# Performance work log

Hardware: AMD Instinct MI355X
Metric: run time of the kernel (lower is better)

## Reference

```python
import jax, jax.numpy as jnp
import numpy as np

N_NODES = 50000; N_INTRA = 800000; N_INTER = 400000; N_IEDGE = 600000
N_GRAPHS = 128; F_IN = 54; DIM = 128; N_GNN = 3; DIM_MLP = 128
DEV_VDW_COEFF = 0.2; EPS_LO = 0.0178; EPS_HI = 0.2
VDW_N_SHORT = 10.0; VDW_N_LONG = 6.0
RANGE_LO = 0.5; RANGE_HI = 5.0
HBOND_CUT = (-0.7, 0.0); METAL_CUT = (-0.7, 0.0); HYDRO_CUT = (0.5, 1.5)


def _lin(key, fi, fo):
    return jax.random.normal(key, (fi, fo), jnp.float32) / np.float32(np.sqrt(fi))


def setup_inputs():
    key = jax.random.key(0)
    ks = iter(jax.random.split(key, 48))
    nk = lambda: next(ks)
    inp = {}
    inp['x'] = jax.random.normal(nk(), (N_NODES, F_IN), jnp.float32)
    inp['pos'] = jax.random.uniform(nk(), (N_NODES, 3), jnp.float32, 0.0, 20.0)
    inp['vdw_radii'] = jax.random.uniform(nk(), (N_NODES,), jnp.float32, 1.0, 2.0)
    inp['rotor'] = jax.random.randint(nk(), (N_GRAPHS, 1), 0, 20).astype(jnp.float32)
    inp['edge_index'] = jax.random.randint(nk(), (2, N_INTRA), 0, N_NODES)
    inp['edge_index_c'] = jax.random.randint(nk(), (2, N_INTER), 0, N_NODES)
    inp['edge_index_i'] = jax.random.randint(nk(), (2, N_IEDGE), 0, N_NODES)
    inp['batch'] = jnp.sort(jax.random.randint(nk(), (N_NODES,), 0, N_GRAPHS))
    for name, p in (('is_metal', 0.02), ('is_h_donor', 0.15), ('is_h_acceptor', 0.2), ('is_hydrophobic', 0.4)):
        inp[name] = jax.random.bernoulli(nk(), p, (N_NODES,))
    inp['embed_W'] = _lin(nk(), F_IN, DIM)
    inp['gat_W'] = jax.random.normal(nk(), (N_GNN, DIM, DIM), jnp.float32) / np.float32(np.sqrt(DIM))
    inp['gat_Wb'] = jnp.zeros((N_GNN, DIM), jnp.float32)
    inp['gat_A'] = 0.1 * jax.random.normal(nk(), (N_GNN, DIM, DIM), jnp.float32) / np.float32(np.sqrt(DIM))
    inp['gat_gate_w'] = jax.random.normal(nk(), (N_GNN, 2 * DIM, 1), jnp.float32) / np.float32(np.sqrt(2 * DIM))
    inp['gat_gate_b'] = jnp.zeros((N_GNN, 1), jnp.float32)
    inp['inter_W'] = jax.random.normal(nk(), (N_GNN, DIM, DIM), jnp.float32) / np.float32(np.sqrt(DIM))
    inp['inter_Wb'] = jnp.zeros((N_GNN, DIM), jnp.float32)
    inp['inter_gate_w'] = jax.random.normal(nk(), (N_GNN, 2 * DIM, 1), jnp.float32) / np.float32(np.sqrt(2 * DIM))
    inp['inter_gate_b'] = jnp.zeros((N_GNN, 1), jnp.float32)
    inp['eps_w1'] = _lin(nk(), 2 * DIM, DIM_MLP); inp['eps_b1'] = jnp.zeros((DIM_MLP,), jnp.float32)
    inp['eps_w2'] = _lin(nk(), DIM_MLP, 1); inp['eps_b2'] = jnp.zeros((1,), jnp.float32)
    inp['dvdw_w1'] = _lin(nk(), 2 * DIM, DIM_MLP); inp['dvdw_b1'] = jnp.zeros((DIM_MLP,), jnp.float32)
    inp['dvdw_w2'] = _lin(nk(), DIM_MLP, 1); inp['dvdw_b2'] = jnp.zeros((1,), jnp.float32)
    inp['hbond_coeff'] = jnp.array([1.0], jnp.float32)
    inp['hydrophobic_coeff'] = jnp.array([0.5], jnp.float32)
    inp['rotor_coeff'] = jnp.array([0.5], jnp.float32)
    return inp


def _gated_gat(x, src, dst, W, Wb, A, gw, gb):
    n = x.shape[0]
    h = x @ W + Wb                                   # [N, D]
    logits = jnp.sum((h @ A)[dst] * h[src], axis=-1)  # per-edge attention logit
    mx = jax.ops.segment_max(logits, dst, num_segments=n)
    mx = jnp.where(jnp.isfinite(mx), mx, 0.0)
    ex = jnp.exp(logits - mx[dst])
    den = jax.ops.segment_sum(ex, dst, num_segments=n)
    alpha = ex / (den[dst] + 1e-16)                  # segment softmax over incoming edges
    h_prime = jax.nn.relu(jax.ops.segment_sum(alpha[:, None] * h[src], dst, num_segments=n))
    z = jax.nn.sigmoid(jnp.concatenate([x, h_prime], -1) @ gw + gb)
    return z * x + (1.0 - z) * h_prime


def _interaction(x, src, dst, W, Wb, gw, gb):
    n = x.shape[0]
    m = jax.ops.segment_sum(jax.nn.relu(x[src] @ W + Wb), dst, num_segments=n)
    z = jax.nn.sigmoid(jnp.concatenate([x, m], -1) @ gw + gb)
    return z * x + (1.0 - z) * m


def _lj(D, R, eps, n_short, n_long):
    dr = jnp.maximum(D / R, 0.5)  # numerical clamp mirroring PIGNet's distance clamp
    n = jnp.where(dr < 1.0, n_short, n_long)
    return eps * (dr ** (-2.0 * n) - 2.0 * dr ** (-n))


def _linear_potential(D, R, minima, c_short, c_long):
    frac = jnp.clip(((D - R) - c_long) / (c_short - c_long), 0.0, 1.0)
    return minima * frac


def _forward(x, pos, vdw_radii, rotor, embed_W, gat_W, gat_Wb, gat_A, gat_gate_w, gat_gate_b,
             inter_W, inter_Wb, inter_gate_w, inter_gate_b,
             eps_w1, eps_b1, eps_w2, eps_b2, dvdw_w1, dvdw_b1, dvdw_w2, dvdw_b2,
             hbond_coeff, hydrophobic_coeff, rotor_coeff,
             edge_index, edge_index_c, edge_index_i, batch,
             is_metal, is_h_donor, is_h_acceptor, is_hydrophobic):
    h = x @ embed_W
    for l in range(N_GNN):
        h = _gated_gat(h, edge_index[0], edge_index[1], gat_W[l], gat_Wb[l], gat_A[l], gat_gate_w[l], gat_gate_b[l])
    for l in range(N_GNN):
        h = _interaction(h, edge_index_c[0], edge_index_c[1], inter_W[l], inter_Wb[l], inter_gate_w[l], inter_gate_b[l])
    i, j = edge_index_i[0], edge_index_i[1]
    diff = pos[i] - pos[j]
    D = jnp.sqrt(jnp.sum(diff * diff, axis=-1) + 1e-10)           # [E]
    rmask = ((D >= RANGE_LO) & (D <= RANGE_HI)).astype(h.dtype)
    x_cat = jnp.concatenate([h[i], h[j]], axis=-1)                # [E, 2*DIM]
    dvdw = jnp.tanh(jax.nn.relu(x_cat @ dvdw_w1 + dvdw_b1) @ dvdw_w2 + dvdw_b2)[:, 0]
    dvdw = dvdw * DEV_VDW_COEFF * rmask
    R = vdw_radii[i] + vdw_radii[j] + dvdw
    eps = jax.nn.sigmoid(jax.nn.relu(x_cat @ eps_w1 + eps_b1) @ eps_w2 + eps_b2)[:, 0]
    eps = eps * (EPS_HI - EPS_LO) + EPS_LO
    min_hb = -hbond_coeff ** 2
    min_hp = -hydrophobic_coeff ** 2
    e = jnp.stack([
        _lj(D, R, eps, VDW_N_SHORT, VDW_N_LONG),
        _linear_potential(D, R, min_hb, *HBOND_CUT),
        _linear_potential(D, R, min_hb, *METAL_CUT),
        _linear_potential(D, R, min_hp, *HYDRO_CUT),
    ])                                                            # [4, E]
    no_metal = ~(is_metal[i] | is_metal[j])
    masks = jnp.stack([
        no_metal,
        ((is_h_donor[i] & is_h_acceptor[j]) | (is_h_acceptor[i] & is_h_donor[j])) & no_metal,
        (is_metal[i] & is_h_acceptor[j]) | (is_h_acceptor[i] & is_metal[j]),
        is_hydrophobic[i] & is_hydrophobic[j] & no_metal,
    ]).astype(e.dtype)
    e = e * masks * rmask
    energies = jax.ops.segment_sum(e.T, batch[i], num_segments=N_GRAPHS)  # [G, 4]
    penalty = 1.0 + rotor_coeff ** 2 * rotor                               # [G, 1]
    return energies / penalty, dvdw


def reference(x, pos, vdw_radii, rotor, edge_index, edge_index_c, edge_index_i, batch,
              is_metal, is_h_donor, is_h_acceptor, is_hydrophobic,
              embed_W, gat_W, gat_Wb, gat_A, gat_gate_w, gat_gate_b,
              inter_W, inter_Wb, inter_gate_w, inter_gate_b,
              eps_w1, eps_b1, eps_w2, eps_b2, dvdw_w1, dvdw_b1, dvdw_w2, dvdw_b2,
              hbond_coeff, hydrophobic_coeff, rotor_coeff):
    return _forward(x, pos, vdw_radii, rotor, embed_W, gat_W, gat_Wb, gat_A, gat_gate_w, gat_gate_b,
                    inter_W, inter_Wb, inter_gate_w, inter_gate_b,
                    eps_w1, eps_b1, eps_w2, eps_b2, dvdw_w1, dvdw_b1, dvdw_w2, dvdw_b2,
                    hbond_coeff, hydrophobic_coeff, rotor_coeff,
                    edge_index, edge_index_c, edge_index_i, batch,
                    is_metal, is_h_donor, is_h_acceptor, is_hydrophobic)
```

## Files before the change

### kernel.cpp

```cpp
#include <hip/hip_runtime.h>
#include <math.h>

#define NN 50000
#define EA 800000
#define EC 400000
#define EIN 600000
#define NG 128
#define FIN 54

#define DEV_VDW 0.2f
#define EPS_LO_ 0.0178f
#define EPS_HI_ 0.2f

typedef unsigned int uint;
typedef unsigned short ushort;
typedef __attribute__((ext_vector_type(8))) short bf16x8;
typedef __attribute__((ext_vector_type(4))) float f32x4;

__device__ __forceinline__ ushort f2bf(float f){
  uint x = __float_as_uint(f);
  uint r = x + 0x7fffu + ((x >> 16) & 1u);
  return (ushort)(r >> 16);
}
__device__ __forceinline__ uint f2bf2(float a, float b){
  return (uint)f2bf(a) | ((uint)f2bf(b) << 16);
}
__device__ __forceinline__ void decode8(uint4 u, float* f){
  f[0] = __uint_as_float(u.x << 16); f[1] = __uint_as_float(u.x & 0xffff0000u);
  f[2] = __uint_as_float(u.y << 16); f[3] = __uint_as_float(u.y & 0xffff0000u);
  f[4] = __uint_as_float(u.z << 16); f[5] = __uint_as_float(u.z & 0xffff0000u);
  f[6] = __uint_as_float(u.w << 16); f[7] = __uint_as_float(u.w & 0xffff0000u);
}

__global__ void k_count2(const int* __restrict__ dstA, const int* __restrict__ dstC,
                         int* __restrict__ cntA, int* __restrict__ cntC){
  int half = blockIdx.x >= 1024;
  const int* dst = half ? dstC : dstA;
  int* cnt = half ? cntC : cntA;
  int E = half ? EC : EA;
  int bid = blockIdx.x - (half ? 1024 : 0);
  int i = bid * 256 + threadIdx.x;
  for (; i < E; i += 1024 * 256) atomicAdd(&cnt[dst[i]], 1);
}

__global__ void k_scan2(const int* __restrict__ cntA, int* __restrict__ offA, int* __restrict__ curA,
                        const int* __restrict__ cntC, int* __restrict__ offC, int* __restrict__ curC){
  const int* cnt = blockIdx.x ? cntC : cntA;
  int* off = blockIdx.x ? offC : offA;
  int* cur = blockIdx.x ? curC : curA;
  int n = NN;
  __shared__ int wsums[16];
  __shared__ int run_s;
  int tid = threadIdx.x;
  int lane = tid & 63, w = tid >> 6;
  if (tid == 0) run_s = 0;
  __syncthreads();
  for (int base = 0; base < n; base += 1024){
    int run = run_s;
    int i = base + tid;
    int v = (i < n) ? cnt[i] : 0;
    int s = v;
    #pragma unroll
    for (int o = 1; o < 64; o <<= 1){ int t = __shfl_up(s, o, 64); if (lane >= o) s += t; }
    if (lane == 63) wsums[w] = s;
    __syncthreads();
    if (w == 0 && lane < 16){
      int t = wsums[lane];
      #pragma unroll
      for (int o = 1; o < 16; o <<= 1){ int u = __shfl_up(t, o, 64); if (lane >= o) t += u; }
      wsums[lane] = t;
    }
    __syncthreads();
    int woff = (w == 0) ? 0 : wsums[w - 1];
    int excl = run + woff + (s - v);
    if (i < n){ off[i] = excl; cur[i] = excl; }
    int tot = wsums[15];
    __syncthreads();
    if (tid == 0) run_s = run + tot;
    __syncthreads();
  }
  if (threadIdx.x == 0) off[n] = run_s;
}

__global__ void k_place2(const int* __restrict__ eiA, const int* __restrict__ eiC,
                         int* __restrict__ curA, int* __restrict__ srcA,
                         int* __restrict__ curC, int* __restrict__ srcC){
  int half = blockIdx.x >= 1024;
  const int* src = half ? eiC : eiA;
  const int* dst = half ? eiC + EC : eiA + EA;
  int* cur = half ? curC : curA;
  int* outp = half ? srcC : srcA;
  int E = half ? EC : EA;
  int bid = blockIdx.x - (half ? 1024 : 0);
  int i = bid * 256 + threadIdx.x;
  for (; i < E; i += 1024 * 256){
    int d = dst[i];
    int slot = atomicAdd(&cur[d], 1);
    outp[slot] = src[i];
  }
}

__global__ void k_nodeinfo(const float* __restrict__ POS, const float* __restrict__ RAD,
                           const int* __restrict__ Mmet, const int* __restrict__ Mdon,
                           const int* __restrict__ Macc, const int* __restrict__ Mhyd,
                           const int* __restrict__ BATCH,
                           float4* __restrict__ PRAD, uint* __restrict__ MB){
  int n = blockIdx.x * 256 + threadIdx.x;
  if (n < NN){
    PRAD[n] = make_float4(POS[3*n], POS[3*n+1], POS[3*n+2], RAD[n]);
    uint m = (Mmet[n] ? 1u : 0u) | (Mdon[n] ? 2u : 0u) | (Macc[n] ? 4u : 0u) |
             (Mhyd[n] ? 8u : 0u) | ((uint)BATCH[n] << 8);
    MB[n] = m;
  }
}

__global__ __launch_bounds__(256) void k_prepw(const float* __restrict__ gatW, const float* __restrict__ gatA,
                        const float* __restrict__ intW, const float* __restrict__ dw1,
                        const float* __restrict__ ew1,
                        const float* __restrict__ gatWb, const float* __restrict__ intWb,
                        const float* __restrict__ db1, const float* __restrict__ eb1,
                        uint* __restrict__ Wt, float* __restrict__ BIASALL){
  __shared__ ushort L[128 * 132];
  int m = blockIdx.x;
  int tid = threadIdx.x;
  if (m == 13){
    for (int idx = tid; idx < 13 * 128; idx += 256){
      int slot = idx >> 7, c = idx & 127;
      if (slot >= 3 && slot < 6) continue;
      float v = 0.f;
      if (slot < 3) v = gatWb[slot * 128 + c];
      else if (slot < 9) v = intWb[(slot - 6) * 128 + c];
      else if (slot == 9) v = db1[c];
      else if (slot == 11) v = eb1[c];
      BIASALL[idx] = v;
    }
    return;
  }
  if (m >= 3 && m < 6){
    int l = m - 3;
    const float* Wf  = gatW + l * 16384;
    const float* Af  = gatA + l * 16384;
    const float* Wbf = gatWb + l * 128;
    for (int idx = tid; idx < 16384; idx += 256){
      int k = idx >> 7, n = idx & 127;
      L[k * 132 + n] = f2bf(Af[idx]);
    }
    __syncthreads();
    int r = tid >> 1, ch = tid & 1;
    float accv[64];
    #pragma unroll
    for (int c = 0; c < 64; ++c) accv[c] = 0.f;
    float accb = 0.f;
    int bc = tid & 127;
    for (int mm = 0; mm < 128; ++mm){
      float wv = Wf[r * 128 + mm];
      const uint* Lr32 = (const uint*)&L[mm * 132 + ch * 64];
      #pragma unroll
      for (int c2 = 0; c2 < 32; ++c2){
        uint u = Lr32[c2];
        accv[2 * c2]     += wv * __uint_as_float(u << 16);
        accv[2 * c2 + 1] += wv * __uint_as_float(u & 0xffff0000u);
      }
      accb += Wbf[mm] * __uint_as_float((uint)L[mm * 132 + bc] << 16);
    }
    __syncthreads();
    #pragma unroll
    for (int c = 0; c < 64; ++c) L[r * 132 + ch * 64 + c] = f2bf(accv[c]);
    if (tid < 128) BIASALL[(3 + l) * 128 + tid] = accb;
    __syncthreads();
    int n = tid & 127, half = tid >> 7;
    uint* outp = Wt + (size_t)m * 8192 + n * 64 + half * 32;
    #pragma unroll
    for (int kk2 = 0; kk2 < 32; ++kk2){
      int k = half * 64 + 2 * kk2;
      uint u = (uint)L[k * 132 + n] | ((uint)L[(k + 1) * 132 + n] << 16);
      outp[kk2] = u;
    }
    return;
  }
  const float* src = (m < 3)  ? gatW + m * 16384 :
                     (m < 9)  ? intW + (m - 6) * 16384 :
                     (m < 11) ? dw1 + (m - 9) * 16384 :
                                ew1 + (m - 11) * 16384;
  for (int idx = tid; idx < 16384; idx += 256){
    int k = idx >> 7, n = idx & 127;
    L[k * 132 + n] = f2bf(src[idx]);
  }
  __syncthreads();
  int n = tid & 127, half = tid >> 7;
  uint* outp = Wt + (size_t)m * 8192 + n * 64 + half * 32;
  #pragma unroll
  for (int kk2 = 0; kk2 < 32; ++kk2){
    int k = half * 64 + 2 * kk2;
    uint u = (uint)L[k * 132 + n] | ((uint)L[(k + 1) * 132 + n] << 16);
    outp[kk2] = u;
  }
}

__global__ void k_embed(const float* __restrict__ X, const float* __restrict__ W,
                        float* __restrict__ H, uint* __restrict__ Hh){
  __shared__ float Wls[FIN * 128];
  int tid = threadIdx.x;
  for (int i = tid; i < FIN * 128; i += 128) Wls[i] = W[i];
  __syncthreads();
  for (int row = blockIdx.x; row < NN; row += gridDim.x){
    const float* xr = X + row * FIN;
    float acc = 0.f;
    #pragma unroll
    for (int k = 0; k < FIN; ++k) acc += xr[k] * Wls[k * 128 + tid];
    H[(size_t)row * 128 + tid] = acc;
    ((ushort*)Hh)[(size_t)row * 128 + tid] = f2bf(acc);
  }
}

template<bool RELU>
__global__ __launch_bounds__(256) void k_gemm_mfma(const uint* __restrict__ Ah,
        const uint* __restrict__ Bt0, size_t strideB,
        const float* __restrict__ bias0, size_t strideBias,
        uint* __restrict__ C0, size_t strideC, int N){
  const uint* Bt = Bt0 + (size_t)blockIdx.y * strideB;
  const float* bias = bias0 + (size_t)blockIdx.y * strideBias;
  uint* Cout = C0 + (size_t)blockIdx.y * strideC;
  int tid = threadIdx.x;
  int lane = tid & 63;
  int wv = tid >> 6;
  int row0 = blockIdx.x * 128 + wv * 32;
  int l15 = lane & 15, lg = lane >> 4;
  int ra0 = row0 + l15, ra1 = row0 + 16 + l15;
  const uint* pa0 = Ah + (size_t)(ra0 < N ? ra0 : 0) * 64 + lg * 4;
  const uint* pa1 = Ah + (size_t)(ra1 < N ? ra1 : 0) * 64 + lg * 4;
  const uint* pb  = Bt + (size_t)l15 * 64 + lg * 4;
  f32x4 acc[2][8] = {};
  #pragma unroll
  for (int c = 0; c < 4; ++c){
    bf16x8 a0 = *(const bf16x8*)(pa0 + c * 16);
    bf16x8 a1 = *(const bf16x8*)(pa1 + c * 16);
    #pragma unroll
    for (int ct = 0; ct < 8; ++ct){
      bf16x8 b = *(const bf16x8*)(pb + ct * 1024 + c * 16);
      acc[0][ct] = __builtin_amdgcn_mfma_f32_16x16x32_bf16(a0, b, acc[0][ct], 0, 0, 0);
      acc[1][ct] = __builtin_amdgcn_mfma_f32_16x16x32_bf16(a1, b, acc[1][ct], 0, 0, 0);
    }
  }
  #pragma unroll
  for (int ct = 0; ct < 8; ++ct){
    int col = ct * 16 + l15;
    float bv = bias[col];
    #pragma unroll
    for (int rt = 0; rt < 2; ++rt){
      int rbase = row0 + rt * 16 + lg * 4;
      f32x4 a4 = acc[rt][ct];
      #pragma unroll
      for (int r = 0; r < 4; ++r){
        int row = rbase + r;
        if (row < N){
          float t = a4[r] + bv;
          if (RELU) t = fmaxf(t, 0.f);
          ((ushort*)Cout)[(size_t)row * 128 + col] = f2bf(t);
        }
      }
    }
  }
}

__global__ __launch_bounds__(256) void k_gat(float* __restrict__ H, uint* __restrict__ Hh,
                      const uint* __restrict__ HWh, const uint* __restrict__ HAh,
                      const int* __restrict__ off, const int* __restrict__ srcs,
                      const float* __restrict__ GW, const float* __restrict__ GB){
  int tid = threadIdx.x;
  int n = blockIdx.x * 4 + (tid >> 6);
  if (n >= NN) return;
  int lane = tid & 63;
  int sub = lane & 15;
  int grp = lane >> 4;
  uint4 au = *(const uint4*)(HAh + (size_t)n * 64 + sub * 4);
  float a[8]; decode8(au, a);
  int e0 = off[n], deg = off[n + 1] - e0;
  float m = -1e30f, den = 0.f;
  float acc[8] = {};
  int slot = grp;
  bool act = slot < deg;
  int sv = (sub == 0 && act) ? srcs[e0 + slot] : 0;
  int s = __shfl(sv, lane & 48);
  uint4 wu = {};
  if (act) wu = *(const uint4*)(HWh + (size_t)s * 64 + sub * 4);
  int nit = (deg + 3) >> 2;
  for (int t = 0; t < nit; ++t){
    int slotn = slot + 4;
    bool actn = slotn < deg;
    int svn = (sub == 0 && actn) ? srcs[e0 + slotn] : 0;
    int sn = __shfl(svn, lane & 48);
    uint4 wun = {};
    if (actn) wun = *(const uint4*)(HWh + (size_t)sn * 64 + sub * 4);
    float w[8]; decode8(wu, w);
    float p = a[0]*w[0] + a[1]*w[1] + a[2]*w[2] + a[3]*w[3]
            + a[4]*w[4] + a[5]*w[5] + a[6]*w[6] + a[7]*w[7];
    #pragma unroll
    for (int o = 8; o; o >>= 1) p += __shfl_xor(p, o, 64);
    if (act){
      float mn = fmaxf(m, p);
      float cf = __expf(m - mn);
      float ex = __expf(p - mn);
      den = den * cf + ex;
      #pragma unroll
      for (int q = 0; q < 8; ++q) acc[q] = acc[q] * cf + ex * w[q];
      m = mn;
    }
    slot = slotn; act = actn; wu = wun;
  }
  #pragma unroll
  for (int o = 16; o <= 32; o <<= 1){
    float mo  = __shfl_xor(m, o, 64);
    float dno = __shfl_xor(den, o, 64);
    float ao[8];
    #pragma unroll
    for (int q = 0; q < 8; ++q) ao[q] = __shfl_xor(acc[q], o, 64);
    float mn = fmaxf(m, mo);
    float cf = __expf(m - mn), cfo = __expf(mo - mn);
    den = den * cf + dno * cfo;
    #pragma unroll
    for (int q = 0; q < 8; ++q) acc[q] = acc[q] * cf + ao[q] * cfo;
    m = mn;
  }
  float inv = 1.f / (den + 1e-16f);
  float hp[8];
  #pragma unroll
  for (int q = 0; q < 8; ++q) hp[q] = fmaxf(acc[q] * inv, 0.f);
  float x[8];
  *(float4*)&x[0] = *(const float4*)(H + (size_t)n * 128 + sub * 8);
  *(float4*)&x[4] = *(const float4*)(H + (size_t)n * 128 + sub * 8 + 4);
  float gx[8], gh[8];
  *(float4*)&gx[0] = *(const float4*)(GW + sub * 8);
  *(float4*)&gx[4] = *(const float4*)(GW + sub * 8 + 4);
  *(float4*)&gh[0] = *(const float4*)(GW + 128 + sub * 8);
  *(float4*)&gh[4] = *(const float4*)(GW + 128 + sub * 8 + 4);
  float g = 0.f;
  #pragma unroll
  for (int q = 0; q < 8; ++q) g += x[q] * gx[q] + hp[q] * gh[q];
  #pragma unroll
  for (int o = 8; o; o >>= 1) g += __shfl_xor(g, o, 64);
  g += GB[0];
  float z = 1.f / (1.f + __expf(-g));
  #pragma unroll
  for (int q = 0; q < 8; ++q) x[q] = z * x[q] + (1.f - z) * hp[q];
  if (grp == 0){
    *(float4*)(H + (size_t)n * 128 + sub * 8)     = *(float4*)&x[0];
    *(float4*)(H + (size_t)n * 128 + sub * 8 + 4) = *(float4*)&x[4];
    uint4 hw;
    hw.x = f2bf2(x[0], x[1]); hw.y = f2bf2(x[2], x[3]);
    hw.z = f2bf2(x[4], x[5]); hw.w = f2bf2(x[6], x[7]);
    *(uint4*)(Hh + (size_t)n * 64 + sub * 4) = hw;
  }
}

__global__ __launch_bounds__(256) void k_inter(float* __restrict__ H, uint* __restrict__ Hh,
                        const uint* __restrict__ Th,
                        const int* __restrict__ off, const int* __restrict__ srcs,
                        const float* __restrict__ GW, const float* __restrict__ GB){
  int tid = threadIdx.x;
  int n = blockIdx.x * 4 + (tid >> 6);
  if (n >= NN) return;
  int lane = tid & 63;
  int sub = lane & 15;
  int grp = lane >> 4;
  int e0 = off[n], deg = off[n + 1] - e0;
  float acc[8] = {};
  int slot = grp;
  bool act = slot < deg;
  int sv = (sub == 0 && act) ? srcs[e0 + slot] : 0;
  int s = __shfl(sv, lane & 48);
  uint4 wu = {};
  if (act) wu = *(const uint4*)(Th + (size_t)s * 64 + sub * 4);
  int nit = (deg + 3) >> 2;
  for (int t = 0; t < nit; ++t){
    int slotn = slot + 4;
    bool actn = slotn < deg;
    int svn = (sub == 0 && actn) ? srcs[e0 + slotn] : 0;
    int sn = __shfl(svn, lane & 48);
    uint4 wun = {};
    if (actn) wun = *(const uint4*)(Th + (size_t)sn * 64 + sub * 4);
    if (act){
      float w[8]; decode8(wu, w);
      #pragma unroll
      for (int q = 0; q < 8; ++q) acc[q] += w[q];
    }
    slot = slotn; act = actn; wu = wun;
  }
  #pragma unroll
  for (int q = 0; q < 8; ++q){
    acc[q] += __shfl_xor(acc[q], 16, 64);
    acc[q] += __shfl_xor(acc[q], 32, 64);
  }
  float x[8];
  *(float4*)&x[0] = *(const float4*)(H + (size_t)n * 128 + sub * 8);
  *(float4*)&x[4] = *(const float4*)(H + (size_t)n * 128 + sub * 8 + 4);
  float gx[8], gh[8];
  *(float4*)&gx[0] = *(const float4*)(GW + sub * 8);
  *(float4*)&gx[4] = *(const float4*)(GW + sub * 8 + 4);
  *(float4*)&gh[0] = *(const float4*)(GW + 128 + sub * 8);
  *(float4*)&gh[4] = *(const float4*)(GW + 128 + sub * 8 + 4);
  float g = 0.f;
  #pragma unroll
  for (int q = 0; q < 8; ++q) g += x[q] * gx[q] + acc[q] * gh[q];
  #pragma unroll
  for (int o = 8; o; o >>= 1) g += __shfl_xor(g, o, 64);
  g += GB[0];
  float z = 1.f / (1.f + __expf(-g));
  #pragma unroll
  for (int q = 0; q < 8; ++q) x[q] = z * x[q] + (1.f - z) * acc[q];
  if (grp == 0){
    *(float4*)(H + (size_t)n * 128 + sub * 8)     = *(float4*)&x[0];
    *(float4*)(H + (size_t)n * 128 + sub * 8 + 4) = *(float4*)&x[4];
    uint4 hw;
    hw.x = f2bf2(x[0], x[1]); hw.y = f2bf2(x[2], x[3]);
    hw.z = f2bf2(x[4], x[5]); hw.w = f2bf2(x[6], x[7]);
    *(uint4*)(Hh + (size_t)n * 64 + sub * 4) = hw;
  }
}

__global__ __launch_bounds__(256) void k_edges(
    const int* __restrict__ EI,
    const float4* __restrict__ PRAD, const uint* __restrict__ MB,
    const uint* __restrict__ Pd, const uint* __restrict__ Qd,
    const uint* __restrict__ Pe, const uint* __restrict__ Qe,
    const float* __restrict__ w2d, const float* __restrict__ b2d,
    const float* __restrict__ w2e, const float* __restrict__ b2e,
    const float* __restrict__ hbc, const float* __restrict__ hpc,
    float* __restrict__ geng, float* __restrict__ outdv){
  __shared__ float eg[NG * 4];
  int tid = threadIdx.x;
  for (int i = tid; i < NG * 4; i += 256) eg[i] = 0.f;
  __syncthreads();
  int sub = tid & 15;
  int gid = blockIdx.x * 16 + (tid >> 4);
  int ngrp = gridDim.x * 16;
  float wdv[8], wev[8];
  *(float4*)&wdv[0] = *(const float4*)(w2d + sub * 8);
  *(float4*)&wdv[4] = *(const float4*)(w2d + sub * 8 + 4);
  *(float4*)&wev[0] = *(const float4*)(w2e + sub * 8);
  *(float4*)&wev[4] = *(const float4*)(w2e + sub * 8 + 4);
  float bd = b2d[0], be = b2e[0];
  float minhb = -hbc[0] * hbc[0], minhp = -hpc[0] * hpc[0];

  int e = gid;
  uint4 pd0 = {}, qd0 = {}, pe0 = {}, qe0 = {};
  float4 pri0 = {}, prj0 = {};
  uint mbi0 = 0, mbj0 = 0;
  int i1 = 0, j1 = 0;
  if (e < EIN){
    int i0 = EI[e], j0 = EI[EIN + e];
    pd0 = *(const uint4*)(Pd + (size_t)i0 * 64 + sub * 4);
    qd0 = *(const uint4*)(Qd + (size_t)j0 * 64 + sub * 4);
    pe0 = *(const uint4*)(Pe + (size_t)i0 * 64 + sub * 4);
    qe0 = *(const uint4*)(Qe + (size_t)j0 * 64 + sub * 4);
    pri0 = PRAD[i0]; prj0 = PRAD[j0]; mbi0 = MB[i0]; mbj0 = MB[j0];
  }
  if (e + ngrp < EIN){ i1 = EI[e + ngrp]; j1 = EI[EIN + e + ngrp]; }

  for (; e < EIN; e += ngrp){
    uint4 pd1 = {}, qd1 = {}, pe1 = {}, qe1 = {};
    float4 pri1 = {}, prj1 = {};
    uint mbi1 = 0, mbj1 = 0;
    int i2 = 0, j2 = 0;
    if (e + ngrp < EIN){
      pd1 = *(const uint4*)(Pd + (size_t)i1 * 64 + sub * 4);
      qd1 = *(const uint4*)(Qd + (size_t)j1 * 64 + sub * 4);
      pe1 = *(const uint4*)(Pe + (size_t)i1 * 64 + sub * 4);
      qe1 = *(const uint4*)(Qe + (size_t)j1 * 64 + sub * 4);
      pri1 = PRAD[i1]; prj1 = PRAD[j1]; mbi1 = MB[i1]; mbj1 = MB[j1];
    }
    if (e + 2 * ngrp < EIN){ i2 = EI[e + 2 * ngrp]; j2 = EI[EIN + e + 2 * ngrp]; }

    float pdf[8], qdf[8], pef[8], qef[8];
    decode8(pd0, pdf); decode8(qd0, qdf); decode8(pe0, pef); decode8(qe0, qef);
    float sd = 0.f, se = 0.f;
    #pragma unroll
    for (int q = 0; q < 8; ++q){
      sd += fmaxf(pdf[q] + qdf[q], 0.f) * wdv[q];
      se += fmaxf(pef[q] + qef[q], 0.f) * wev[q];
    }
    #pragma unroll
    for (int o = 8; o; o >>= 1){
      sd += __shfl_xor(sd, o, 64);
      se += __shfl_xor(se, o, 64);
    }
    sd += bd; se += be;
    float dx = pri0.x - prj0.x, dy = pri0.y - prj0.y, dz = pri0.z - prj0.z;
    float D = sqrtf(dx * dx + dy * dy + dz * dz + 1e-10f);
    float rmask = (D >= 0.5f && D <= 5.0f) ? 1.f : 0.f;
    float ex2 = __expf(2.f * fminf(sd, 15.f));
    float th = __fdividef(ex2 - 1.f, ex2 + 1.f);
    float dvdw = th * DEV_VDW * rmask;
    float eps = __fdividef(1.f, 1.f + __expf(-se)) * (EPS_HI_ - EPS_LO_) + EPS_LO_;
    float R = pri0.w + prj0.w + dvdw;
    float dr = fmaxf(__fdividef(D, R), 0.5f);
    float nn2 = (dr < 1.f) ? 10.f : 6.f;
    float tp = __expf(-nn2 * __logf(dr));
    float ev = eps * (tp * tp - 2.f * tp);
    float dmr = D - R;
    float f1 = fminf(fmaxf(dmr * (-1.f / 0.7f), 0.f), 1.f);
    float f3 = fminf(fmaxf(1.5f - dmr, 0.f), 1.f);
    bool metI = mbi0 & 1, metJ = mbj0 & 1;
    bool donI = mbi0 & 2, donJ = mbj0 & 2;
    bool accI = mbi0 & 4, accJ = mbj0 & 4;
    bool hyI  = mbi0 & 8, hyJ  = mbj0 & 8;
    bool nm = !(metI || metJ);
    float E0 = nm ? ev * rmask : 0.f;
    float E1 = (((donI && accJ) || (accI && donJ)) && nm) ? minhb * f1 * rmask : 0.f;
    float E2 = ((metI && accJ) || (accI && metJ)) ? minhb * f1 * rmask : 0.f;
    float E3 = (hyI && hyJ && nm) ? minhp * f3 * rmask : 0.f;
    if (sub == 0){
      outdv[e] = dvdw;
      int g = (int)(mbi0 >> 8) * 4;
      atomicAdd(&eg[g + 0], E0);
      atomicAdd(&eg[g + 1], E1);
      atomicAdd(&eg[g + 2], E2);
      atomicAdd(&eg[g + 3], E3);
    }
    pd0 = pd1; qd0 = qd1; pe0 = pe1; qe0 = qe1;
    pri0 = pri1; prj0 = prj1; mbi0 = mbi1; mbj0 = mbj1;
    i1 = i2; j1 = j2;
  }
  __syncthreads();
  float* part = geng + (size_t)(blockIdx.x & 7) * (NG * 4);
  for (int i2 = tid; i2 < NG * 4; i2 += 256) atomicAdd(&part[i2], eg[i2]);
}

__global__ void k_final(const float* __restrict__ geng, const float* __restrict__ rotor,
                        const float* __restrict__ rc, float* __restrict__ out){
  int t = blockIdx.x * blockDim.x + threadIdx.x;
  if (t < NG * 4){
    int g = t >> 2;
    float s = 0.f;
    #pragma unroll
    for (int p = 0; p < 8; ++p) s += geng[p * NG * 4 + t];
    float pen = 1.f + rc[0] * rc[0] * rotor[g];
    out[t] = s / pen;
  }
}

extern "C" void kernel_launch(void* const* d_in, const int* in_sizes, int n_in,
                              void* d_out, int out_size, void* d_ws, size_t ws_size,
                              hipStream_t stream){
  (void)in_sizes; (void)n_in; (void)out_size; (void)ws_size;
  const float* X    = (const float*)d_in[0];
  const float* POS  = (const float*)d_in[1];
  const float* RAD  = (const float*)d_in[2];
  const float* ROT  = (const float*)d_in[3];
  const int* EIa    = (const int*)d_in[4];
  const int* EIc    = (const int*)d_in[5];
  const int* EIi    = (const int*)d_in[6];
  const int* BATCH  = (const int*)d_in[7];
  const int* Mmet = (const int*)d_in[8];
  const int* Mdon = (const int*)d_in[9];
  const int* Macc = (const int*)d_in[10];
  const int* Mhyd = (const int*)d_in[11];
  const float* embW  = (const float*)d_in[12];
  const float* gatW  = (const float*)d_in[13];
  const float* gatWb = (const float*)d_in[14];
  const float* gatA  = (const float*)d_in[15];
  const float* gatGw = (const float*)d_in[16];
  const float* gatGb = (const float*)d_in[17];
  const float* intW  = (const float*)d_in[18];
  const float* intWb = (const float*)d_in[19];
  const float* intGw = (const float*)d_in[20];
  const float* intGb = (const float*)d_in[21];
  const float* ew1 = (const float*)d_in[22];
  const float* eb1 = (const float*)d_in[23];
  const float* ew2 = (const float*)d_in[24];
  const float* eb2 = (const float*)d_in[25];
  const float* dw1 = (const float*)d_in[26];
  const float* db1 = (const float*)d_in[27];
  const float* dw2 = (const float*)d_in[28];
  const float* db2 = (const float*)d_in[29];
  const float* hbc = (const float*)d_in[30];
  const float* hpc = (const float*)d_in[31];
  const float* rcc = (const float*)d_in[32];
  float* out = (float*)d_out;

  char* w = (char*)d_ws;
  float* H   = (float*)w; w += (size_t)NN * 128 * 4;
  uint* Hh   = (uint*)w;  w += (size_t)NN * 64 * 4;
  uint* BAh  = (uint*)w;  w += (size_t)NN * 64 * 4;
  uint* BBh  = (uint*)w;  w += (size_t)NN * 64 * 4;
  uint* Peh  = (uint*)w;  w += (size_t)NN * 64 * 4;
  uint* Qeh  = (uint*)w;  w += (size_t)NN * 64 * 4;
  uint* WT   = (uint*)w;  w += (size_t)13 * 8192 * 4;
  float* BIASALL = (float*)w; w += (size_t)13 * 128 * 4;
  float4* PRAD = (float4*)w; w += (size_t)NN * 16;
  uint* MBb  = (uint*)w;  w += (size_t)NN * 4;
  float* GENG = (float*)w; w += (size_t)8 * 512 * 4;
  int* cntA = (int*)w; w += (size_t)NN * 4;
  int* offA = (int*)w; w += (size_t)(NN + 1) * 4;
  int* curA = (int*)w; w += (size_t)NN * 4;
  int* srcA = (int*)w; w += (size_t)EA * 4;
  int* cntC = (int*)w; w += (size_t)NN * 4;
  int* offC = (int*)w; w += (size_t)(NN + 1) * 4;
  int* curC = (int*)w; w += (size_t)NN * 4;
  int* srcC = (int*)w; w += (size_t)EC * 4;
  uint* Th  = BAh;
  uint* Pdh = BAh;
  uint* Qdh = BBh;

  hipMemsetAsync(cntA, 0, (size_t)NN * 4, stream);
  hipMemsetAsync(cntC, 0, (size_t)NN * 4, stream);
  hipMemsetAsync(GENG, 0, (size_t)8 * 512 * 4, stream);

  k_count2<<<2048, 256, 0, stream>>>(EIa + EA, EIc + EC, cntA, cntC);
  k_scan2<<<2, 1024, 0, stream>>>(cntA, offA, curA, cntC, offC, curC);
  k_place2<<<2048, 256, 0, stream>>>(EIa, EIc, curA, srcA, curC, srcC);

  k_prepw<<<14, 256, 0, stream>>>(gatW, gatA, intW, dw1, ew1, gatWb, intWb, db1, eb1, WT, BIASALL);
  k_nodeinfo<<<(NN + 255) / 256, 256, 0, stream>>>(POS, RAD, Mmet, Mdon, Macc, Mhyd, BATCH, PRAD, MBb);
  k_embed<<<2048, 128, 0, stream>>>(X, embW, H, Hh);

  int gg = (NN + 127) / 128;
  int nodeGrid = (NN + 3) / 4;
  for (int l = 0; l < 3; ++l){
    k_gemm_mfma<false><<<dim3(gg, 2), 256, 0, stream>>>(Hh, WT + (size_t)l * 8192, (size_t)3 * 8192,
                                                        BIASALL + l * 128, (size_t)3 * 128,
                                                        BAh, (size_t)NN * 64, NN);
    k_gat<<<nodeGrid, 256, 0, stream>>>(H, Hh, BAh, BBh, offA, srcA, gatGw + l * 256, gatGb + l);
  }
  for (int l = 0; l < 3; ++l){
    k_gemm_mfma<true><<<dim3(gg, 1), 256, 0, stream>>>(Hh, WT + (size_t)(6 + l) * 8192, 0,
                                                       BIASALL + (6 + l) * 128, 0, Th, 0, NN);
    k_inter<<<nodeGrid, 256, 0, stream>>>(H, Hh, Th, offC, srcC, intGw + l * 256, intGb + l);
  }
  k_gemm_mfma<false><<<dim3(gg, 4), 256, 0, stream>>>(Hh, WT + (size_t)9 * 8192, (size_t)8192,
                                                      BIASALL + 9 * 128, (size_t)128,
                                                      BAh, (size_t)NN * 64, NN);

  k_edges<<<2048, 256, 0, stream>>>(EIi, PRAD, MBb, Pdh, Qdh, Peh, Qeh,
                                    dw2, db2, ew2, eb2, hbc, hpc,
                                    GENG, out + 512);
  k_final<<<2, 256, 0, stream>>>(GENG, ROT, rcc, out);
}
```

Baseline: 894.0 us.

## Use 16-lane node groups for GAT/inter and CSR-sort interaction edges

The GAT and inter kernels now give each node a 16-lane group instead of a 64-lane wavefront. Each group walks its neighbours serially with a two-deep prefetch, which removes the cross-group online-softmax merge and the idle lanes on low-degree nodes. The interaction edges are also bucketed into CSR by source node, with the original edge ids stored alongside. The edge kernel can then load source features once per node and accumulate energies in registers before doing a few global atomics, where it used to do per-edge shared atomics. The cost is an extra count/scan/place pass over the interaction edges and a scattered dvdw write through the edge-id indirection.

```diff
diff --git a/kernel.cpp b/kernel.cpp
--- a/kernel.cpp
+++ b/kernel.cpp
@@ -32,22 +32,23 @@
   f[6] = __uint_as_float(u.w << 16); f[7] = __uint_as_float(u.w & 0xffff0000u);
 }
 
-__global__ void k_count2(const int* __restrict__ dstA, const int* __restrict__ dstC,
-                         int* __restrict__ cntA, int* __restrict__ cntC){
-  int half = blockIdx.x >= 1024;
-  const int* dst = half ? dstC : dstA;
-  int* cnt = half ? cntC : cntA;
-  int E = half ? EC : EA;
-  int bid = blockIdx.x - (half ? 1024 : 0);
-  int i = bid * 256 + threadIdx.x;
-  for (; i < E; i += 1024 * 256) atomicAdd(&cnt[dst[i]], 1);
-}
-
-__global__ void k_scan2(const int* __restrict__ cntA, int* __restrict__ offA, int* __restrict__ curA,
-                        const int* __restrict__ cntC, int* __restrict__ offC, int* __restrict__ curC){
-  const int* cnt = blockIdx.x ? cntC : cntA;
-  int* off = blockIdx.x ? offC : offA;
-  int* cur = blockIdx.x ? curC : curA;
+__global__ void k_count3(const int* __restrict__ dstA, const int* __restrict__ dstC,
+                         const int* __restrict__ dstI,
+                         int* __restrict__ cntA, int* __restrict__ cntC, int* __restrict__ cntI){
+  int b = blockIdx.x;
+  const int* dst; int* cnt; int E; int bid; int nb;
+  if (b < 1024){ dst = dstA; cnt = cntA; E = EA;  bid = b;        nb = 1024; }
+  else if (b < 1536){ dst = dstC; cnt = cntC; E = EC;  bid = b - 1024; nb = 512; }
+  else { dst = dstI; cnt = cntI; E = EIN; bid = b - 1536; nb = 1024; }
+  for (int i = bid * 256 + threadIdx.x; i < E; i += nb * 256) atomicAdd(&cnt[dst[i]], 1);
+}
+
+__global__ void k_scan3(const int* __restrict__ cntA, int* __restrict__ offA, int* __restrict__ curA,
+                        const int* __restrict__ cntC, int* __restrict__ offC, int* __restrict__ curC,
+                        const int* __restrict__ cntI, int* __restrict__ offI, int* __restrict__ curI){
+  const int* cnt = (blockIdx.x == 0) ? cntA : (blockIdx.x == 1) ? cntC : cntI;
+  int* off = (blockIdx.x == 0) ? offA : (blockIdx.x == 1) ? offC : offI;
+  int* cur = (blockIdx.x == 0) ? curA : (blockIdx.x == 1) ? curC : curI;
   int n = NN;
   __shared__ int wsums[16];
   __shared__ int run_s;
@@ -82,21 +83,33 @@
   if (threadIdx.x == 0) off[n] = run_s;
 }
 
-__global__ void k_place2(const int* __restrict__ eiA, const int* __restrict__ eiC,
+__global__ void k_place3(const int* __restrict__ eiA, const int* __restrict__ eiC,
+                         const int* __restrict__ eiI,
                          int* __restrict__ curA, int* __restrict__ srcA,
-                         int* __restrict__ curC, int* __restrict__ srcC){
-  int half = blockIdx.x >= 1024;
-  const int* src = half ? eiC : eiA;
-  const int* dst = half ? eiC + EC : eiA + EA;
-  int* cur = half ? curC : curA;
-  int* outp = half ? srcC : srcA;
-  int E = half ? EC : EA;
-  int bid = blockIdx.x - (half ? 1024 : 0);
-  int i = bid * 256 + threadIdx.x;
-  for (; i < E; i += 1024 * 256){
-    int d = dst[i];
-    int slot = atomicAdd(&cur[d], 1);
-    outp[slot] = src[i];
+                         int* __restrict__ curC, int* __restrict__ srcC,
+                         int* __restrict__ curI, int* __restrict__ srcI, int* __restrict__ eidI){
+  int b = blockIdx.x;
+  if (b < 1024){
+    for (int i = b * 256 + threadIdx.x; i < EA; i += 1024 * 256){
+      int d = eiA[EA + i];
+      int slot = atomicAdd(&curA[d], 1);
+      srcA[slot] = eiA[i];
+    }
+  } else if (b < 1536){
+    int bid = b - 1024;
+    for (int i = bid * 256 + threadIdx.x; i < EC; i += 512 * 256){
+      int d = eiC[EC + i];
+      int slot = atomicAdd(&curC[d], 1);
+      srcC[slot] = eiC[i];
+    }
+  } else {
+    int bid = b - 1536;
+    for (int i = bid * 256 + threadIdx.x; i < EIN; i += 1024 * 256){
+      int key = eiI[i];
+      int slot = atomicAdd(&curI[key], 1);
+      srcI[slot] = eiI[EIN + i];
+      eidI[slot] = i;
+    }
   }
 }
 
@@ -268,59 +281,33 @@
                       const int* __restrict__ off, const int* __restrict__ srcs,
                       const float* __restrict__ GW, const float* __restrict__ GB){
   int tid = threadIdx.x;
-  int n = blockIdx.x * 4 + (tid >> 6);
+  int sub = tid & 15;
+  int n = blockIdx.x * 16 + (tid >> 4);
   if (n >= NN) return;
-  int lane = tid & 63;
-  int sub = lane & 15;
-  int grp = lane >> 4;
   uint4 au = *(const uint4*)(HAh + (size_t)n * 64 + sub * 4);
   float a[8]; decode8(au, a);
   int e0 = off[n], deg = off[n + 1] - e0;
-  float m = -1e30f, den = 0.f;
+  float m = -INFINITY, den = 0.f;
   float acc[8] = {};
-  int slot = grp;
-  bool act = slot < deg;
-  int sv = (sub == 0 && act) ? srcs[e0 + slot] : 0;
-  int s = __shfl(sv, lane & 48);
-  uint4 wu = {};
-  if (act) wu = *(const uint4*)(HWh + (size_t)s * 64 + sub * 4);
-  int nit = (deg + 3) >> 2;
-  for (int t = 0; t < nit; ++t){
-    int slotn = slot + 4;
-    bool actn = slotn < deg;
-    int svn = (sub == 0 && actn) ? srcs[e0 + slotn] : 0;
-    int sn = __shfl(svn, lane & 48);
-    uint4 wun = {};
-    if (actn) wun = *(const uint4*)(HWh + (size_t)sn * 64 + sub * 4);
-    float w[8]; decode8(wu, w);
+  uint4 w0v = {}, w1v = {};
+  if (deg > 0) w0v = *(const uint4*)(HWh + (size_t)srcs[e0] * 64 + sub * 4);
+  if (deg > 1) w1v = *(const uint4*)(HWh + (size_t)srcs[e0 + 1] * 64 + sub * 4);
+  for (int t = 0; t < deg; ++t){
+    uint4 wn = {};
+    if (t + 2 < deg) wn = *(const uint4*)(HWh + (size_t)srcs[e0 + t + 2] * 64 + sub * 4);
+    float w[8]; decode8(w0v, w);
     float p = a[0]*w[0] + a[1]*w[1] + a[2]*w[2] + a[3]*w[3]
             + a[4]*w[4] + a[5]*w[5] + a[6]*w[6] + a[7]*w[7];
     #pragma unroll
     for (int o = 8; o; o >>= 1) p += __shfl_xor(p, o, 64);
-    if (act){
-      float mn = fmaxf(m, p);
-      float cf = __expf(m - mn);
-      float ex = __expf(p - mn);
-      den = den * cf + ex;
-      #pragma unroll
-      for (int q = 0; q < 8; ++q) acc[q] = acc[q] * cf + ex * w[q];
-      m = mn;
-    }
-    slot = slotn; act = actn; wu = wun;
-  }
-  #pragma unroll
-  for (int o = 16; o <= 32; o <<= 1){
-    float mo  = __shfl_xor(m, o, 64);
-    float dno = __shfl_xor(den, o, 64);
-    float ao[8];
-    #pragma unroll
-    for (int q = 0; q < 8; ++q) ao[q] = __shfl_xor(acc[q], o, 64);
-    float mn = fmaxf(m, mo);
-    float cf = __expf(m - mn), cfo = __expf(mo - mn);
-    den = den * cf + dno * cfo;
-    #pragma unroll
-    for (int q = 0; q < 8; ++q) acc[q] = acc[q] * cf + ao[q] * cfo;
+    float mn = fmaxf(m, p);
+    float cf = __expf(m - mn);
+    float ex = __expf(p - mn);
+    den = den * cf + ex;
+    #pragma unroll
+    for (int q = 0; q < 8; ++q) acc[q] = acc[q] * cf + ex * w[q];
     m = mn;
+    w0v = w1v; w1v = wn;
   }
   float inv = 1.f / (den + 1e-16f);
   float hp[8];
@@ -343,14 +330,12 @@
   float z = 1.f / (1.f + __expf(-g));
   #pragma unroll
   for (int q = 0; q < 8; ++q) x[q] = z * x[q] + (1.f - z) * hp[q];
-  if (grp == 0){
-    *(float4*)(H + (size_t)n * 128 + sub * 8)     = *(float4*)&x[0];
-    *(float4*)(H + (size_t)n * 128 + sub * 8 + 4) = *(float4*)&x[4];
-    uint4 hw;
-    hw.x = f2bf2(x[0], x[1]); hw.y = f2bf2(x[2], x[3]);
-    hw.z = f2bf2(x[4], x[5]); hw.w = f2bf2(x[6], x[7]);
-    *(uint4*)(Hh + (size_t)n * 64 + sub * 4) = hw;
-  }
+  *(float4*)(H + (size_t)n * 128 + sub * 8)     = *(float4*)&x[0];
+  *(float4*)(H + (size_t)n * 128 + sub * 8 + 4) = *(float4*)&x[4];
+  uint4 hw;
+  hw.x = f2bf2(x[0], x[1]); hw.y = f2bf2(x[2], x[3]);
+  hw.z = f2bf2(x[4], x[5]); hw.w = f2bf2(x[6], x[7]);
+  *(uint4*)(Hh + (size_t)n * 64 + sub * 4) = hw;
 }
 
 __global__ __launch_bounds__(256) void k_inter(float* __restrict__ H, uint* __restrict__ Hh,
@@ -358,38 +343,21 @@
                         const int* __restrict__ off, const int* __restrict__ srcs,
                         const float* __restrict__ GW, const float* __restrict__ GB){
   int tid = threadIdx.x;
-  int n = blockIdx.x * 4 + (tid >> 6);
+  int sub = tid & 15;
+  int n = blockIdx.x * 16 + (tid >> 4);
   if (n >= NN) return;
-  int lane = tid & 63;
-  int sub = lane & 15;
-  int grp = lane >> 4;
   int e0 = off[n], deg = off[n + 1] - e0;
   float acc[8] = {};
-  int slot = grp;
-  bool act = slot < deg;
-  int sv = (sub == 0 && act) ? srcs[e0 + slot] : 0;
-  int s = __shfl(sv, lane & 48);
-  uint4 wu = {};
-  if (act) wu = *(const uint4*)(Th + (size_t)s * 64 + sub * 4);
-  int nit = (deg + 3) >> 2;
-  for (int t = 0; t < nit; ++t){
-    int slotn = slot + 4;
-    bool actn = slotn < deg;
-    int svn = (sub == 0 && actn) ? srcs[e0 + slotn] : 0;
-    int sn = __shfl(svn, lane & 48);
-    uint4 wun = {};
-    if (actn) wun = *(const uint4*)(Th + (size_t)sn * 64 + sub * 4);
-    if (act){
-      float w[8]; decode8(wu, w);
-      #pragma unroll
-      for (int q = 0; q < 8; ++q) acc[q] += w[q];
-    }
-    slot = slotn; act = actn; wu = wun;
-  }
-  #pragma unroll
-  for (int q = 0; q < 8; ++q){
-    acc[q] += __shfl_xor(acc[q], 16, 64);
-    acc[q] += __shfl_xor(acc[q], 32, 64);
+  uint4 w0v = {}, w1v = {};
+  if (deg > 0) w0v = *(const uint4*)(Th + (size_t)srcs[e0] * 64 + sub * 4);
+  if (deg > 1) w1v = *(const uint4*)(Th + (size_t)srcs[e0 + 1] * 64 + sub * 4);
+  for (int t = 0; t < deg; ++t){
+    uint4 wn = {};
+    if (t + 2 < deg) wn = *(const uint4*)(Th + (size_t)srcs[e0 + t + 2] * 64 + sub * 4);
+    float w[8]; decode8(w0v, w);
+    #pragma unroll
+    for (int q = 0; q < 8; ++q) acc[q] += w[q];
+    w0v = w1v; w1v = wn;
   }
   float x[8];
   *(float4*)&x[0] = *(const float4*)(H + (size_t)n * 128 + sub * 8);
@@ -408,18 +376,16 @@
   float z = 1.f / (1.f + __expf(-g));
   #pragma unroll
   for (int q = 0; q < 8; ++q) x[q] = z * x[q] + (1.f - z) * acc[q];
-  if (grp == 0){
-    *(float4*)(H + (size_t)n * 128 + sub * 8)     = *(float4*)&x[0];
-    *(float4*)(H + (size_t)n * 128 + sub * 8 + 4) = *(float4*)&x[4];
-    uint4 hw;
-    hw.x = f2bf2(x[0], x[1]); hw.y = f2bf2(x[2], x[3]);
-    hw.z = f2bf2(x[4], x[5]); hw.w = f2bf2(x[6], x[7]);
-    *(uint4*)(Hh + (size_t)n * 64 + sub * 4) = hw;
-  }
+  *(float4*)(H + (size_t)n * 128 + sub * 8)     = *(float4*)&x[0];
+  *(float4*)(H + (size_t)n * 128 + sub * 8 + 4) = *(float4*)&x[4];
+  uint4 hw;
+  hw.x = f2bf2(x[0], x[1]); hw.y = f2bf2(x[2], x[3]);
+  hw.z = f2bf2(x[4], x[5]); hw.w = f2bf2(x[6], x[7]);
+  *(uint4*)(Hh + (size_t)n * 64 + sub * 4) = hw;
 }
 
 __global__ __launch_bounds__(256) void k_edges(
-    const int* __restrict__ EI,
+    const int* __restrict__ offI, const int* __restrict__ srcI, const int* __restrict__ eidI,
     const float4* __restrict__ PRAD, const uint* __restrict__ MB,
     const uint* __restrict__ Pd, const uint* __restrict__ Qd,
     const uint* __restrict__ Pe, const uint* __restrict__ Qe,
@@ -427,13 +393,12 @@
     const float* __restrict__ w2e, const float* __restrict__ b2e,
     const float* __restrict__ hbc, const float* __restrict__ hpc,
     float* __restrict__ geng, float* __restrict__ outdv){
-  __shared__ float eg[NG * 4];
-  int tid = threadIdx.x;
-  for (int i = tid; i < NG * 4; i += 256) eg[i] = 0.f;
-  __syncthreads();
+  int tid = threadIdx.x;
   int sub = tid & 15;
-  int gid = blockIdx.x * 16 + (tid >> 4);
-  int ngrp = gridDim.x * 16;
+  int n = blockIdx.x * 16 + (tid >> 4);
+  if (n >= NN) return;
+  int e0 = offI[n], deg = offI[n + 1] - e0;
+  if (deg == 0) return;
   float wdv[8], wev[8];
   *(float4*)&wdv[0] = *(const float4*)(w2d + sub * 8);
   *(float4*)&wdv[4] = *(const float4*)(w2d + sub * 8 + 4);
@@ -441,38 +406,32 @@
   *(float4*)&wev[4] = *(const float4*)(w2e + sub * 8 + 4);
   float bd = b2d[0], be = b2e[0];
   float minhb = -hbc[0] * hbc[0], minhp = -hpc[0] * hpc[0];
-
-  int e = gid;
-  uint4 pd0 = {}, qd0 = {}, pe0 = {}, qe0 = {};
-  float4 pri0 = {}, prj0 = {};
-  uint mbi0 = 0, mbj0 = 0;
-  int i1 = 0, j1 = 0;
-  if (e < EIN){
-    int i0 = EI[e], j0 = EI[EIN + e];
-    pd0 = *(const uint4*)(Pd + (size_t)i0 * 64 + sub * 4);
-    qd0 = *(const uint4*)(Qd + (size_t)j0 * 64 + sub * 4);
-    pe0 = *(const uint4*)(Pe + (size_t)i0 * 64 + sub * 4);
-    qe0 = *(const uint4*)(Qe + (size_t)j0 * 64 + sub * 4);
-    pri0 = PRAD[i0]; prj0 = PRAD[j0]; mbi0 = MB[i0]; mbj0 = MB[j0];
-  }
-  if (e + ngrp < EIN){ i1 = EI[e + ngrp]; j1 = EI[EIN + e + ngrp]; }
-
-  for (; e < EIN; e += ngrp){
-    uint4 pd1 = {}, qd1 = {}, pe1 = {}, qe1 = {};
-    float4 pri1 = {}, prj1 = {};
-    uint mbi1 = 0, mbj1 = 0;
-    int i2 = 0, j2 = 0;
-    if (e + ngrp < EIN){
-      pd1 = *(const uint4*)(Pd + (size_t)i1 * 64 + sub * 4);
+  uint4 pdu = *(const uint4*)(Pd + (size_t)n * 64 + sub * 4);
+  uint4 peu = *(const uint4*)(Pe + (size_t)n * 64 + sub * 4);
+  float pdf[8], pef[8];
+  decode8(pdu, pdf); decode8(peu, pef);
+  float4 pri = PRAD[n];
+  uint mbi = MB[n];
+  float E0 = 0.f, E1 = 0.f, E2 = 0.f, E3 = 0.f;
+
+  int ee0 = eidI[e0];
+  int j0 = srcI[e0];
+  uint4 qd0 = *(const uint4*)(Qd + (size_t)j0 * 64 + sub * 4);
+  uint4 qe0 = *(const uint4*)(Qe + (size_t)j0 * 64 + sub * 4);
+  float4 prj0 = PRAD[j0];
+  uint mbj0 = MB[j0];
+
+  for (int t = 0; t < deg; ++t){
+    int ee1 = 0; uint4 qd1 = {}, qe1 = {}; float4 prj1 = {}; uint mbj1 = 0;
+    if (t + 1 < deg){
+      int j1 = srcI[e0 + t + 1];
+      ee1 = eidI[e0 + t + 1];
       qd1 = *(const uint4*)(Qd + (size_t)j1 * 64 + sub * 4);
-      pe1 = *(const uint4*)(Pe + (size_t)i1 * 64 + sub * 4);
       qe1 = *(const uint4*)(Qe + (size_t)j1 * 64 + sub * 4);
-      pri1 = PRAD[i1]; prj1 = PRAD[j1]; mbi1 = MB[i1]; mbj1 = MB[j1];
-    }
-    if (e + 2 * ngrp < EIN){ i2 = EI[e + 2 * ngrp]; j2 = EI[EIN + e + 2 * ngrp]; }
-
-    float pdf[8], qdf[8], pef[8], qef[8];
-    decode8(pd0, pdf); decode8(qd0, qdf); decode8(pe0, pef); decode8(qe0, qef);
+      prj1 = PRAD[j1]; mbj1 = MB[j1];
+    }
+    float qdf[8], qef[8];
+    decode8(qd0, qdf); decode8(qe0, qef);
     float sd = 0.f, se = 0.f;
     #pragma unroll
     for (int q = 0; q < 8; ++q){
@@ -485,14 +444,14 @@
       se += __shfl_xor(se, o, 64);
     }
     sd += bd; se += be;
-    float dx = pri0.x - prj0.x, dy = pri0.y - prj0.y, dz = pri0.z - prj0.z;
+    float dx = pri.x - prj0.x, dy = pri.y - prj0.y, dz = pri.z - prj0.z;
     float D = sqrtf(dx * dx + dy * dy + dz * dz + 1e-10f);
     float rmask = (D >= 0.5f && D <= 5.0f) ? 1.f : 0.f;
     float ex2 = __expf(2.f * fminf(sd, 15.f));
     float th = __fdividef(ex2 - 1.f, ex2 + 1.f);
     float dvdw = th * DEV_VDW * rmask;
     float eps = __fdividef(1.f, 1.f + __expf(-se)) * (EPS_HI_ - EPS_LO_) + EPS_LO_;
-    float R = pri0.w + prj0.w + dvdw;
+    float R = pri.w + prj0.w + dvdw;
     float dr = fmaxf(__fdividef(D, R), 0.5f);
     float nn2 = (dr < 1.f) ? 10.f : 6.f;
     float tp = __expf(-nn2 * __logf(dr));
@@ -500,30 +459,26 @@
     float dmr = D - R;
     float f1 = fminf(fmaxf(dmr * (-1.f / 0.7f), 0.f), 1.f);
     float f3 = fminf(fmaxf(1.5f - dmr, 0.f), 1.f);
-    bool metI = mbi0 & 1, metJ = mbj0 & 1;
-    bool donI = mbi0 & 2, donJ = mbj0 & 2;
-    bool accI = mbi0 & 4, accJ = mbj0 & 4;
-    bool hyI  = mbi0 & 8, hyJ  = mbj0 & 8;
+    bool metI = mbi & 1, metJ = mbj0 & 1;
+    bool donI = mbi & 2, donJ = mbj0 & 2;
+    bool accI = mbi & 4, accJ = mbj0 & 4;
+    bool hyI  = mbi & 8, hyJ  = mbj0 & 8;
     bool nm = !(metI || metJ);
-    float E0 = nm ? ev * rmask : 0.f;
-    float E1 = (((donI && accJ) || (accI && donJ)) && nm) ? minhb * f1 * rmask : 0.f;
-    float E2 = ((metI && accJ) || (accI && metJ)) ? minhb * f1 * rmask : 0.f;
-    float E3 = (hyI && hyJ && nm) ? minhp * f3 * rmask : 0.f;
-    if (sub == 0){
-      outdv[e] = dvdw;
-      int g = (int)(mbi0 >> 8) * 4;
-      atomicAdd(&eg[g + 0], E0);
-      atomicAdd(&eg[g + 1], E1);
-      atomicAdd(&eg[g + 2], E2);
-      atomicAdd(&eg[g + 3], E3);
-    }
-    pd0 = pd1; qd0 = qd1; pe0 = pe1; qe0 = qe1;
-    pri0 = pri1; prj0 = prj1; mbi0 = mbi1; mbj0 = mbj1;
-    i1 = i2; j1 = j2;
-  }
-  __syncthreads();
-  float* part = geng + (size_t)(blockIdx.x & 7) * (NG * 4);
-  for (int i2 = tid; i2 < NG * 4; i2 += 256) atomicAdd(&part[i2], eg[i2]);
+    if (sub == 0) outdv[ee0] = dvdw;
+    E0 += nm ? ev * rmask : 0.f;
+    E1 += (((donI && accJ) || (accI && donJ)) && nm) ? minhb * f1 * rmask : 0.f;
+    E2 += ((metI && accJ) || (accI && metJ)) ? minhb * f1 * rmask : 0.f;
+    E3 += (hyI && hyJ && nm) ? minhp * f3 * rmask : 0.f;
+    ee0 = ee1; qd0 = qd1; qe0 = qe1; prj0 = prj1; mbj0 = mbj1;
+  }
+  if (sub == 0){
+    float* part = geng + (size_t)(blockIdx.x & 7) * (NG * 4);
+    int g = (int)(mbi >> 8) * 4;
+    atomicAdd(&part[g + 0], E0);
+    atomicAdd(&part[g + 1], E1);
+    atomicAdd(&part[g + 2], E2);
+    atomicAdd(&part[g + 3], E3);
+  }
 }
 
 __global__ void k_final(const float* __restrict__ geng, const float* __restrict__ rotor,
@@ -598,24 +553,30 @@
   int* offC = (int*)w; w += (size_t)(NN + 1) * 4;
   int* curC = (int*)w; w += (size_t)NN * 4;
   int* srcC = (int*)w; w += (size_t)EC * 4;
+  int* cntI = (int*)w; w += (size_t)NN * 4;
+  int* offI = (int*)w; w += (size_t)(NN + 1) * 4;
+  int* curI = (int*)w; w += (size_t)NN * 4;
+  int* srcI = (int*)w; w += (size_t)EIN * 4;
+  int* eidI = (int*)w; w += (size_t)EIN * 4;
   uint* Th  = BAh;
   uint* Pdh = BAh;
   uint* Qdh = BBh;
 
   hipMemsetAsync(cntA, 0, (size_t)NN * 4, stream);
   hipMemsetAsync(cntC, 0, (size_t)NN * 4, stream);
+  hipMemsetAsync(cntI, 0, (size_t)NN * 4, stream);
   hipMemsetAsync(GENG, 0, (size_t)8 * 512 * 4, stream);
 
-  k_count2<<<2048, 256, 0, stream>>>(EIa + EA, EIc + EC, cntA, cntC);
-  k_scan2<<<2, 1024, 0, stream>>>(cntA, offA, curA, cntC, offC, curC);
-  k_place2<<<2048, 256, 0, stream>>>(EIa, EIc, curA, srcA, curC, srcC);
+  k_count3<<<2560, 256, 0, stream>>>(EIa + EA, EIc + EC, EIi, cntA, cntC, cntI);
+  k_scan3<<<3, 1024, 0, stream>>>(cntA, offA, curA, cntC, offC, curC, cntI, offI, curI);
+  k_place3<<<2560, 256, 0, stream>>>(EIa, EIc, EIi, curA, srcA, curC, srcC, curI, srcI, eidI);
 
   k_prepw<<<14, 256, 0, stream>>>(gatW, gatA, intW, dw1, ew1, gatWb, intWb, db1, eb1, WT, BIASALL);
   k_nodeinfo<<<(NN + 255) / 256, 256, 0, stream>>>(POS, RAD, Mmet, Mdon, Macc, Mhyd, BATCH, PRAD, MBb);
   k_embed<<<2048, 128, 0, stream>>>(X, embW, H, Hh);
 
   int gg = (NN + 127) / 128;
-  int nodeGrid = (NN + 3) / 4;
+  int nodeGrid = (NN + 15) / 16;
   for (int l = 0; l < 3; ++l){
     k_gemm_mfma<false><<<dim3(gg, 2), 256, 0, stream>>>(Hh, WT + (size_t)l * 8192, (size_t)3 * 8192,
                                                         BIASALL + l * 128, (size_t)3 * 128,
@@ -631,8 +592,8 @@
                                                       BIASALL + 9 * 128, (size_t)128,
                                                       BAh, (size_t)NN * 64, NN);
 
-  k_edges<<<2048, 256, 0, stream>>>(EIi, PRAD, MBb, Pdh, Qdh, Peh, Qeh,
-                                    dw2, db2, ew2, eb2, hbc, hpc,
-                                    GENG, out + 512);
+  k_edges<<<nodeGrid, 256, 0, stream>>>(offI, srcI, eidI, PRAD, MBb, Pdh, Qdh, Peh, Qeh,
+                                        dw2, db2, ew2, eb2, hbc, hpc,
+                                        GENG, out + 512);
   k_final<<<2, 256, 0, stream>>>(GENG, ROT, rcc, out);
 }
```

After: 991.2 us. 10.9% more time.
